# Kernel tuning notes

Hardware: AMD Instinct MI355X
Metric: run time of the kernel (lower is better)

Reference implementation:

```python
import jax, jax.numpy as jnp
import numpy as np

NP_CONST = 48.0  # Np in the original code


def dft_matrices(freq=48, time=512):
    # A[t, f] = exp(-2j*pi*t*f/time)/sqrt(time), split into re/im, shape [time, freq]
    t = np.arange(time)[:, None]
    f = np.arange(freq)[None, :]
    ang = -2.0 * np.pi * t * f / time
    scale = 1.0 / np.sqrt(time)
    return (np.cos(ang) * scale).astype(np.float32), (np.sin(ang) * scale).astype(np.float32)


def _mm(xr, xi, wr, wi):
    # complex matmul: (xr + i xi) @ (wr + i wi)
    return xr @ wr - xi @ wi, xr @ wi + xi @ wr


def _act(R, sigma, theta):
    # scaled soft-threshold (standard LAMP shrinkage); returns f and df/dR
    lam = theta[0] * sigma
    mag = jnp.abs(R)
    shr = jnp.maximum(mag - lam, 0.0)
    f = theta[1] * jnp.sign(R) * shr
    df = theta[1] * (mag > lam).astype(R.dtype)
    return f, df


def setup_inputs() -> dict:
    key = jax.random.key(0)
    L, B = 8, 8192
    dre, dim = dft_matrices(48, 512)
    u = jax.random.normal(key, (B, 48, 2), dtype=jnp.float32)
    # per-layer params initialized to the DFT matrices (as in LAMP_layer.__init__)
    A_re = jnp.broadcast_to(jnp.asarray(dre), (L, 512, 48)).copy()
    A_im = jnp.broadcast_to(jnp.asarray(dim), (L, 512, 48)).copy()
    theta = jnp.broadcast_to(jnp.array([1.0, 1.0, -1.0], dtype=jnp.float32), (L, 3)).copy()
    return {"u": u, "A_re": A_re, "A_im": A_im, "theta": theta,
            "DFT_re": jnp.asarray(dre), "DFT_im": jnp.asarray(dim)}


def _lamp_forward(u, A_re, A_im, theta, DFT_re, DFT_im):
    u_re, u_im = u[:, :, 0], u[:, :, 1]          # [B, 48]
    B = u_re.shape[0]
    z_re, z_im = u_re, u_im
    H_re = jnp.zeros((B, 512), dtype=u.dtype)
    H_im = jnp.zeros((B, 512), dtype=u.dtype)

    def layer(carry, params):
        z_re, z_im, H_re, H_im = carry
        Are, Aim, th = params                      # [512,48], [512,48], [3]
        # Z = z @ A.T : [B,48] x [48,512]
        Z_re, Z_im = _mm(z_re, z_im, Are.T, Aim.T)
        R_re = H_re + Z_re
        R_im = H_im + Z_im
        sigma = jnp.sqrt(jnp.sum(z_re * z_re) + jnp.sum(z_im * z_im)) / jnp.sqrt(NP_CONST)
        Hn_re, d_re = _act(R_re, sigma, th)
        Hn_im, d_im = _act(R_im, sigma, th)
        b_re = d_re.sum() / NP_CONST
        b_im = d_im.sum() / NP_CONST
        # h_hat = H_hat @ A : [B,512] x [512,48]
        h_re, h_im = _mm(Hn_re, Hn_im, Are, Aim)
        zn_re = u_re - h_re + b_re * z_re
        zn_im = u_im - h_im + b_im * z_im
        return (zn_re, zn_im, Hn_re, Hn_im), None

    (z_re, z_im, H_re, H_im), _ = jax.lax.scan(layer, (z_re, z_im, H_re, H_im),
                                               (A_re, A_im, theta))
    h_re, h_im = _mm(H_re, H_im, DFT_re, DFT_im)   # [B, 48]
    return jnp.stack((h_re, h_im), axis=2)          # [B, 48, 2]


def reference(u, A_re, A_im, theta, DFT_re, DFT_im):
    return _lamp_forward(u, A_re, A_im, theta, DFT_re, DFT_im)
```

## Files before the change

kernel.cpp:

```cpp
#include <hip/hip_runtime.h>
#include <hip/hip_bf16.h>
#include <math.h>

#define B_   8192
#define F_   48
#define T_   512
#define L_   8
#define NBLK 512
#define THR  512
#define NW   8
#define RPB  16
#define HST  520
#define ZS   52

typedef unsigned short ushort_t;
typedef unsigned int   uint_t;
typedef __attribute__((ext_vector_type(8))) short short8;
typedef __attribute__((ext_vector_type(4))) float f32x4;

#define MFMA(a,b,c) __builtin_amdgcn_mfma_f32_16x16x32_bf16(a,b,c,0,0,0)

__device__ inline ushort_t f2bf(float x) {
    __hip_bfloat16 h = __float2bfloat16(x);
    return *reinterpret_cast<ushort_t*>(&h);
}
__device__ inline float bf2f(ushort_t x) {
    __hip_bfloat16 h;
    *reinterpret_cast<ushort_t*>(&h) = x;
    return __bfloat162float(h);
}
__device__ inline short8 negbf(short8 v) {
    short8 r;
    #pragma unroll
    for (int i = 0; i < 8; ++i) r[i] = v[i] ^ (short)0x8000;
    return r;
}
__device__ inline short8 pack8(float4 a, float4 b) {
    short8 r;
    r[0]=(short)f2bf(a.x); r[1]=(short)f2bf(a.y); r[2]=(short)f2bf(a.z); r[3]=(short)f2bf(a.w);
    r[4]=(short)f2bf(b.x); r[5]=(short)f2bf(b.y); r[6]=(short)f2bf(b.z); r[7]=(short)f2bf(b.w);
    return r;
}

__device__ inline float blk_sum(float v, float* red8) {
    #pragma unroll
    for (int s = 32; s > 0; s >>= 1) v += __shfl_xor(v, s, 64);
    __syncthreads();
    if ((threadIdx.x & 63) == 0) red8[threadIdx.x >> 6] = v;
    __syncthreads();
    float t = 0.f;
    #pragma unroll
    for (int w = 0; w < NW; ++w) t += red8[w];
    return t;
}

__device__ inline void bar_add(uint_t* cnt, int blk) {
    __hip_atomic_fetch_add(&cnt[(blk & 15) * 32], 1u, __ATOMIC_RELEASE, __HIP_MEMORY_SCOPE_AGENT);
}
__device__ inline void bar_wait(uint_t* cnt, uint_t tgt) {
    if (threadIdx.x == 0) {
        for (;;) {
            uint_t s = 0;
            #pragma unroll
            for (int i = 0; i < 16; ++i)
                s += __hip_atomic_load(&cnt[i * 32], __ATOMIC_RELAXED, __HIP_MEMORY_SCOPE_AGENT);
            if (s >= tgt) break;
            __builtin_amdgcn_s_sleep(2);
        }
        (void)__hip_atomic_load(&cnt[0], __ATOMIC_ACQUIRE, __HIP_MEMORY_SCOPE_AGENT);
    }
    __syncthreads();
}
__device__ inline float aload(const float* p) {
    return __hip_atomic_load(p, __ATOMIC_RELAXED, __HIP_MEMORY_SCOPE_AGENT);
}
__device__ inline void astore(float* p, float v) {
    __hip_atomic_store(p, v, __ATOMIC_RELAXED, __HIP_MEMORY_SCOPE_AGENT);
}

__device__ inline uint_t act2(uint_t v, float lam, float th1, float& cnt_) {
    float lo = __uint_as_float(v << 16);
    float hi = __uint_as_float(v & 0xffff0000u);
    float ml = fabsf(lo), mh = fabsf(hi);
    float fl = th1 * copysignf(fmaxf(ml - lam, 0.f), lo);
    float fh = th1 * copysignf(fmaxf(mh - lam, 0.f), hi);
    cnt_ += ((ml > lam) ? 1.f : 0.f) + ((mh > lam) ? 1.f : 0.f);
    return ((uint_t)f2bf(fl)) | (((uint_t)f2bf(fh)) << 16);
}

__global__ __launch_bounds__(256) void k_pre(
    const float* __restrict__ Ar, const float* __restrict__ Ai,
    const float* __restrict__ Dr, const float* __restrict__ Di,
    ushort_t* __restrict__ Afr, ushort_t* __restrict__ Afi,
    ushort_t* __restrict__ Atr, ushort_t* __restrict__ Ati,
    ushort_t* __restrict__ Dfr, ushort_t* __restrict__ Dfi,
    uint_t* __restrict__ cnt)
{
    const int gt = blockIdx.x * 256 + threadIdx.x;
    const int gs = gridDim.x * 256;
    if (gt < 512) cnt[gt] = 0u;
    for (int idx = gt; idx < L_ * 32768; idx += gs) {
        int j = idx & 7, rest = idx >> 3;
        int mm = rest & 15; rest >>= 4;
        int qq = rest & 3;  rest >>= 2;
        int k2 = rest & 1;  rest >>= 1;
        int tile = rest & 31;
        int l = rest >> 5;
        int t = tile * 16 + mm, k = k2 * 32 + qq * 8 + j;
        float vr = 0.f, vi = 0.f;
        if (k < 48) { int g = l * 24576 + t * 48 + k; vr = Ar[g]; vi = Ai[g]; }
        Afr[idx] = f2bf(vr); Afi[idx] = f2bf(vi);
    }
    for (int idx = gt; idx < L_ * 24576; idx += gs) {
        int j = idx & 7, rest = idx >> 3;
        int mm = rest & 15; rest >>= 4;
        int qq = rest & 3;  rest >>= 2;
        int ks = rest & 15; rest >>= 4;
        int ft = rest % 3;
        int l = rest / 3;
        int f = ft * 16 + mm, k = ks * 32 + qq * 8 + j;
        int g = l * 24576 + k * 48 + f;
        Atr[idx] = f2bf(Ar[g]); Ati[idx] = f2bf(Ai[g]);
    }
    for (int idx = gt; idx < 24576; idx += gs) {
        int j = idx & 7, rest = idx >> 3;
        int mm = rest & 15; rest >>= 4;
        int qq = rest & 3;  rest >>= 2;
        int ks = rest & 15;
        int ft = rest >> 4;
        int f = ft * 16 + mm, k = ks * 32 + qq * 8 + j;
        Dfr[idx] = f2bf(Dr[k * 48 + f]); Dfi[idx] = f2bf(Di[k * 48 + f]);
    }
}

__global__ __launch_bounds__(THR, 4) void k_lamp(
    const float* __restrict__ u,
    const ushort_t* __restrict__ Afr, const ushort_t* __restrict__ Afi,
    const ushort_t* __restrict__ Atr, const ushort_t* __restrict__ Ati,
    const ushort_t* __restrict__ Dfr, const ushort_t* __restrict__ Dfi,
    const float* __restrict__ th,
    float* part_sig, float* part_r, float* part_i, uint_t* cnt,
    float* __restrict__ out)
{
    extern __shared__ char dyn[];
    float*    pR   = (float*)dyn;
    float*    pI   = pR + 4 * 3 * 16 * 17;
    float*    zreL = pI + 4 * 3 * 16 * 17;
    float*    zimL = zreL + RPB * ZS;
    float*    red8 = zimL + RPB * ZS;
    ushort_t* HreL = (ushort_t*)(red8 + 16);
    ushort_t* HimL = HreL + RPB * HST;

    const int tid = threadIdx.x, blk = blockIdx.x;
    const int row0 = blk * RPB;
    const int wave = tid >> 6, lane = tid & 63;
    const int quad = lane >> 4, m = lane & 15;
    const int kq = wave;
    const float2* u2 = (const float2*)u;
    uint_t tgt = 0;

    float acc = 0.f;
    #pragma unroll
    for (int k2 = 0; k2 < 2; ++k2) {
        int j = tid + k2 * THR;
        if (j < RPB * F_) {
            int r = j / 48, c = j - r * 48;
            float2 v = u2[(row0 + r) * 48 + c];
            zreL[r * ZS + c] = v.x; zimL[r * ZS + c] = v.y;
            acc += v.x * v.x + v.y * v.y;
        }
    }
    float s0 = blk_sum(acc, red8);
    if (tid == 0) { astore(&part_sig[blk], s0); bar_add(cnt, blk); }
    tgt += NBLK;

    for (int l = 0; l < L_; ++l) {
        const float* zpr = zreL + m * ZS;
        const float* zpi = zimL + m * ZS;
        short8 zr0 = pack8(*(const float4*)(zpr + quad * 8), *(const float4*)(zpr + quad * 8 + 4));
        short8 zi0 = pack8(*(const float4*)(zpi + quad * 8), *(const float4*)(zpi + quad * 8 + 4));
        short8 zr1 = {0,0,0,0,0,0,0,0}, zi1 = {0,0,0,0,0,0,0,0};
        if (quad < 2) {
            zr1 = pack8(*(const float4*)(zpr + 32 + quad * 8), *(const float4*)(zpr + 36 + quad * 8));
            zi1 = pack8(*(const float4*)(zpi + 32 + quad * 8), *(const float4*)(zpi + 36 + quad * 8));
        }
        short8 zin0 = negbf(zi0), zin1 = negbf(zi1);

        const ushort_t* Aflr = Afr + (size_t)l * 32768;
        const ushort_t* Afli = Afi + (size_t)l * 32768;
        #pragma unroll
        for (int ct = 0; ct < 4; ++ct) {
            const int tile = wave * 4 + ct;
            const ushort_t* rp = Aflr + (size_t)(tile * 2) * 512 + lane * 8;
            const ushort_t* ip = Afli + (size_t)(tile * 2) * 512 + lane * 8;
            short8 ar0 = *(const short8*)rp;
            short8 ar1 = *(const short8*)(rp + 512);
            short8 ai0 = *(const short8*)ip;
            short8 ai1 = *(const short8*)(ip + 512);
            f32x4 accR = {0.f,0.f,0.f,0.f}, accI = {0.f,0.f,0.f,0.f};
            accR = MFMA(zr0, ar0, accR);
            accR = MFMA(zr1, ar1, accR);
            accR = MFMA(zin0, ai0, accR);
            accR = MFMA(zin1, ai1, accR);
            accI = MFMA(zr0, ai0, accI);
            accI = MFMA(zr1, ai1, accI);
            accI = MFMA(zi0, ar0, accI);
            accI = MFMA(zi1, ar1, accI);
            const int t = tile * 16 + m;
            #pragma unroll
            for (int reg = 0; reg < 4; ++reg) {
                const int lr = quad * 4 + reg;
                float Rr = accR[reg], Ri = accI[reg];
                if (l > 0) { Rr += bf2f(HreL[lr * HST + t]); Ri += bf2f(HimL[lr * HST + t]); }
                HreL[lr * HST + t] = f2bf(Rr);
                HimL[lr * HST + t] = f2bf(Ri);
            }
        }

        bar_wait(cnt, tgt);
        float ssum = blk_sum(aload(&part_sig[tid]), red8);
        const float lam = th[l * 3] * sqrtf(ssum * (1.0f / 48.0f));
        const float th1 = th[l * 3 + 1];

        float cr = 0.f, ci = 0.f;
        uint4* Hr4 = (uint4*)HreL;
        uint4* Hi4 = (uint4*)HimL;
        #pragma unroll
        for (int k2 = 0; k2 < 2; ++k2) {
            int j = tid + k2 * THR;
            int r = j >> 6, c4 = j & 63;
            uint4* pr = Hr4 + r * 65 + c4;
            uint4* pi = Hi4 + r * 65 + c4;
            uint4 xr = *pr, xi = *pi;
            xr.x = act2(xr.x, lam, th1, cr); xr.y = act2(xr.y, lam, th1, cr);
            xr.z = act2(xr.z, lam, th1, cr); xr.w = act2(xr.w, lam, th1, cr);
            xi.x = act2(xi.x, lam, th1, ci); xi.y = act2(xi.y, lam, th1, ci);
            xi.z = act2(xi.z, lam, th1, ci); xi.w = act2(xi.w, lam, th1, ci);
            *pr = xr; *pi = xi;
        }

        if (l == L_ - 1) { __syncthreads(); break; }

        float csr = blk_sum(cr, red8);
        if (tid == 0) astore(&part_r[blk], csr);
        float csi = blk_sum(ci, red8);
        if (tid == 0) { astore(&part_i[blk], csi); bar_add(cnt, blk); }
        tgt += NBLK;

        const ushort_t* Atlr = Atr + (size_t)l * 24576;
        const ushort_t* Atli = Ati + (size_t)l * 24576;
        f32x4 aR[3], aI[3];
        #pragma unroll
        for (int q = 0; q < 3; ++q) { aR[q] = (f32x4){0,0,0,0}; aI[q] = (f32x4){0,0,0,0}; }
        #pragma unroll
        for (int ks = 0; ks < 2; ++ks) {
            const int ksa = kq * 2 + ks;
            const int k0 = ksa * 32 + quad * 8;
            short8 hr = *(const short8*)&HreL[m * HST + k0];
            short8 hi = *(const short8*)&HimL[m * HST + k0];
            short8 hin = negbf(hi);
            #pragma unroll
            for (int ft = 0; ft < 3; ++ft) {
                short8 br = *(const short8*)(Atlr + (size_t)((ft * 16 + ksa) * 64 + lane) * 8);
                short8 bi = *(const short8*)(Atli + (size_t)((ft * 16 + ksa) * 64 + lane) * 8);
                aR[ft] = MFMA(hr, br, aR[ft]);
                aR[ft] = MFMA(hin, bi, aR[ft]);
                aI[ft] = MFMA(hr, bi, aI[ft]);
                aI[ft] = MFMA(hi, br, aI[ft]);
            }
        }
        {
            const int s = kq & 3;
            if (kq < 4) {
                #pragma unroll
                for (int ft = 0; ft < 3; ++ft)
                    #pragma unroll
                    for (int reg = 0; reg < 4; ++reg) {
                        pR[((s * 3 + ft) * 16 + quad * 4 + reg) * 17 + m] = aR[ft][reg];
                        pI[((s * 3 + ft) * 16 + quad * 4 + reg) * 17 + m] = aI[ft][reg];
                    }
            }
            __syncthreads();
            if (kq >= 4) {
                #pragma unroll
                for (int ft = 0; ft < 3; ++ft)
                    #pragma unroll
                    for (int reg = 0; reg < 4; ++reg) {
                        pR[((s * 3 + ft) * 16 + quad * 4 + reg) * 17 + m] += aR[ft][reg];
                        pI[((s * 3 + ft) * 16 + quad * 4 + reg) * 17 + m] += aI[ft][reg];
                    }
            }
        }

        bar_wait(cnt, tgt);
        float bsr = blk_sum(aload(&part_r[tid]), red8);
        float bsi = blk_sum(aload(&part_i[tid]), red8);
        const float bre = th1 * bsr * (1.0f / 48.0f);
        const float bim = th1 * bsi * (1.0f / 48.0f);

        float nrm = 0.f;
        #pragma unroll
        for (int k2 = 0; k2 < 2; ++k2) {
            int j = tid + k2 * THR;
            if (j < RPB * F_) {
                int r = j / 48, f = j - r * 48;
                int lr = r & 15, ft = f >> 4, c = f & 15;
                float hR = 0.f, hI = 0.f;
                #pragma unroll
                for (int q = 0; q < 4; ++q) {
                    hR += pR[((q * 3 + ft) * 16 + lr) * 17 + c];
                    hI += pI[((q * 3 + ft) * 16 + lr) * 17 + c];
                }
                float2 uv = u2[(row0 + r) * 48 + f];
                float zr = zreL[r * ZS + f], zi = zimL[r * ZS + f];
                float znr = uv.x - hR + bre * zr;
                float zni = uv.y - hI + bim * zi;
                zreL[r * ZS + f] = znr; zimL[r * ZS + f] = zni;
                nrm += znr * znr + zni * zni;
            }
        }
        float ns = blk_sum(nrm, red8);
        if (tid == 0) { astore(&part_sig[blk], ns); bar_add(cnt, blk); }
        tgt += NBLK;
    }

    f32x4 fR[3], fI[3];
    #pragma unroll
    for (int q = 0; q < 3; ++q) { fR[q] = (f32x4){0,0,0,0}; fI[q] = (f32x4){0,0,0,0}; }
    #pragma unroll
    for (int ks = 0; ks < 2; ++ks) {
        const int ksa = kq * 2 + ks;
        const int k0 = ksa * 32 + quad * 8;
        short8 hr = *(const short8*)&HreL[m * HST + k0];
        short8 hi = *(const short8*)&HimL[m * HST + k0];
        short8 hin = negbf(hi);
        #pragma unroll
        for (int ft = 0; ft < 3; ++ft) {
            short8 br = *(const short8*)(Dfr + (size_t)((ft * 16 + ksa) * 64 + lane) * 8);
            short8 bi = *(const short8*)(Dfi + (size_t)((ft * 16 + ksa) * 64 + lane) * 8);
            fR[ft] = MFMA(hr, br, fR[ft]);
            fR[ft] = MFMA(hin, bi, fR[ft]);
            fI[ft] = MFMA(hr, bi, fI[ft]);
            fI[ft] = MFMA(hi, br, fI[ft]);
        }
    }
    {
        const int s = kq & 3;
        if (kq < 4) {
            #pragma unroll
            for (int ft = 0; ft < 3; ++ft)
                #pragma unroll
                for (int reg = 0; reg < 4; ++reg) {
                    pR[((s * 3 + ft) * 16 + quad * 4 + reg) * 17 + m] = fR[ft][reg];
                    pI[((s * 3 + ft) * 16 + quad * 4 + reg) * 17 + m] = fI[ft][reg];
                }
        }
        __syncthreads();
        if (kq >= 4) {
            #pragma unroll
            for (int ft = 0; ft < 3; ++ft)
                #pragma unroll
                for (int reg = 0; reg < 4; ++reg) {
                    pR[((s * 3 + ft) * 16 + quad * 4 + reg) * 17 + m] += fR[ft][reg];
                    pI[((s * 3 + ft) * 16 + quad * 4 + reg) * 17 + m] += fI[ft][reg];
                }
        }
    }
    __syncthreads();
    float2* out2 = (float2*)out;
    #pragma unroll
    for (int k2 = 0; k2 < 2; ++k2) {
        int j = tid + k2 * THR;
        if (j < RPB * F_) {
            int r = j / 48, f = j - r * 48;
            int lr = r & 15, ft = f >> 4, c = f & 15;
            float hR = 0.f, hI = 0.f;
            #pragma unroll
            for (int q = 0; q < 4; ++q) {
                hR += pR[((q * 3 + ft) * 16 + lr) * 17 + c];
                hI += pI[((q * 3 + ft) * 16 + lr) * 17 + c];
            }
            out2[(row0 + r) * 48 + f] = make_float2(hR, hI);
        }
    }
}

extern "C" void kernel_launch(void* const* d_in, const int* in_sizes, int n_in,
                              void* d_out, int out_size, void* d_ws, size_t ws_size,
                              hipStream_t stream) {
    (void)in_sizes; (void)n_in; (void)out_size; (void)ws_size;
    const float* u  = (const float*)d_in[0];
    const float* Ar = (const float*)d_in[1];
    const float* Ai = (const float*)d_in[2];
    const float* th = (const float*)d_in[3];
    const float* Dr = (const float*)d_in[4];
    const float* Di = (const float*)d_in[5];
    float* out = (float*)d_out;

    char* p = (char*)d_ws;
    auto alloc = [&](size_t bytes) -> char* {
        char* r = p;
        p += (bytes + 255) & ~(size_t)255;
        return r;
    };
    float*    part_sig = (float*)alloc(NBLK * 4);
    float*    part_r   = (float*)alloc(NBLK * 4);
    float*    part_i   = (float*)alloc(NBLK * 4);
    uint_t*   cnt      = (uint_t*)alloc(512 * 4);
    ushort_t* Afr = (ushort_t*)alloc((size_t)L_ * 32768 * 2);
    ushort_t* Afi = (ushort_t*)alloc((size_t)L_ * 32768 * 2);
    ushort_t* Atr = (ushort_t*)alloc((size_t)L_ * 24576 * 2);
    ushort_t* Ati = (ushort_t*)alloc((size_t)L_ * 24576 * 2);
    ushort_t* Dfr = (ushort_t*)alloc((size_t)24576 * 2);
    ushort_t* Dfi = (ushort_t*)alloc((size_t)24576 * 2);

    k_pre<<<256, 256, 0, stream>>>(Ar, Ai, Dr, Di, Afr, Afi, Atr, Ati, Dfr, Dfi, cnt);

    const uint_t lds_bytes = 66112;
    hipFuncSetAttribute((const void*)k_lamp,
                        hipFuncAttributeMaxDynamicSharedMemorySize, (int)lds_bytes);
    void* args[] = { (void*)&u, (void*)&Afr, (void*)&Afi, (void*)&Atr, (void*)&Ati,
                     (void*)&Dfr, (void*)&Dfi, (void*)&th,
                     (void*)&part_sig, (void*)&part_r, (void*)&part_i,
                     (void*)&cnt, (void*)&out };
    hipLaunchCooperativeKernel((void*)k_lamp, dim3(NBLK), dim3(THR), args,
                               lds_bytes, stream);
}
```

Baseline: 309.5 us.

## Merge per-layer grid barriers by computing next sigma algebraically from partial sums

Removes one of the two grid-wide barriers per layer. Each block now publishes the partial sums of d^2, d·z and z^2 together with the derivative counts, and every block expands the next-layer norm of z = d + b*z from those scalars. The forward GEMM for layer 0 runs before the first barrier wait, and the block size is halved to 256 threads with 4 waves, each handling twice the tiles, so two blocks fit per CU. The trade-offs are less intra-block parallelism and a small rounding difference because the norm is computed from expanded sums instead of directly.

Measured after the change: 292.1 us. 1.06x faster.

```diff
diff --git a/kernel.cpp b/kernel.cpp
--- a/kernel.cpp
+++ b/kernel.cpp
@@ -7,8 +7,8 @@
 #define T_   512
 #define L_   8
 #define NBLK 512
-#define THR  512
-#define NW   8
+#define THR  256
+#define NW   4
 #define RPB  16
 #define HST  520
 #define ZS   52
@@ -42,16 +42,17 @@
     return r;
 }
 
-__device__ inline float blk_sum(float v, float* red8) {
+template<int NQ>
+__device__ inline void reduce_vals(float* v, float* redL, int wave, int lane) {
     #pragma unroll
-    for (int s = 32; s > 0; s >>= 1) v += __shfl_xor(v, s, 64);
+    for (int s = 32; s > 0; s >>= 1)
+        #pragma unroll
+        for (int q = 0; q < NQ; ++q) v[q] += __shfl_xor(v[q], s, 64);
     __syncthreads();
-    if ((threadIdx.x & 63) == 0) red8[threadIdx.x >> 6] = v;
+    if (lane == 0)
+        #pragma unroll
+        for (int q = 0; q < NQ; ++q) redL[q * NW + wave] = v[q];
     __syncthreads();
-    float t = 0.f;
-    #pragma unroll
-    for (int w = 0; w < NW; ++w) t += red8[w];
-    return t;
 }
 
 __device__ inline void bar_add(uint_t* cnt, int blk) {
@@ -133,22 +134,67 @@
     }
 }
 
-__global__ __launch_bounds__(THR, 4) void k_lamp(
+__device__ inline void fwd_gemm(const ushort_t* Aflr, const ushort_t* Afli,
+    const float* zreL, const float* zimL, ushort_t* HreL, ushort_t* HimL,
+    int wave, int lane, int quad, int m, bool addH)
+{
+    const float* zpr = zreL + m * ZS;
+    const float* zpi = zimL + m * ZS;
+    short8 zr0 = pack8(*(const float4*)(zpr + quad * 8), *(const float4*)(zpr + quad * 8 + 4));
+    short8 zi0 = pack8(*(const float4*)(zpi + quad * 8), *(const float4*)(zpi + quad * 8 + 4));
+    short8 zr1 = {0,0,0,0,0,0,0,0}, zi1 = {0,0,0,0,0,0,0,0};
+    if (quad < 2) {
+        zr1 = pack8(*(const float4*)(zpr + 32 + quad * 8), *(const float4*)(zpr + 36 + quad * 8));
+        zi1 = pack8(*(const float4*)(zpi + 32 + quad * 8), *(const float4*)(zpi + 36 + quad * 8));
+    }
+    short8 zin0 = negbf(zi0), zin1 = negbf(zi1);
+    #pragma unroll
+    for (int ct = 0; ct < 8; ++ct) {
+        const int tile = wave * 8 + ct;
+        const ushort_t* rp = Aflr + (size_t)(tile * 2) * 512 + lane * 8;
+        const ushort_t* ip = Afli + (size_t)(tile * 2) * 512 + lane * 8;
+        short8 ar0 = *(const short8*)rp;
+        short8 ar1 = *(const short8*)(rp + 512);
+        short8 ai0 = *(const short8*)ip;
+        short8 ai1 = *(const short8*)(ip + 512);
+        f32x4 accR = {0.f,0.f,0.f,0.f}, accI = {0.f,0.f,0.f,0.f};
+        accR = MFMA(zr0, ar0, accR);
+        accR = MFMA(zr1, ar1, accR);
+        accR = MFMA(zin0, ai0, accR);
+        accR = MFMA(zin1, ai1, accR);
+        accI = MFMA(zr0, ai0, accI);
+        accI = MFMA(zr1, ai1, accI);
+        accI = MFMA(zi0, ar0, accI);
+        accI = MFMA(zi1, ar1, accI);
+        const int t = tile * 16 + m;
+        #pragma unroll
+        for (int reg = 0; reg < 4; ++reg) {
+            const int lr = quad * 4 + reg;
+            float Rr = accR[reg], Ri = accI[reg];
+            if (addH) { Rr += bf2f(HreL[lr * HST + t]); Ri += bf2f(HimL[lr * HST + t]); }
+            HreL[lr * HST + t] = f2bf(Rr);
+            HimL[lr * HST + t] = f2bf(Ri);
+        }
+    }
+    __syncthreads();
+}
+
+__global__ __launch_bounds__(THR, 2) void k_lamp(
     const float* __restrict__ u,
     const ushort_t* __restrict__ Afr, const ushort_t* __restrict__ Afi,
     const ushort_t* __restrict__ Atr, const ushort_t* __restrict__ Ati,
     const ushort_t* __restrict__ Dfr, const ushort_t* __restrict__ Dfi,
     const float* __restrict__ th,
-    float* part_sig, float* part_r, float* part_i, uint_t* cnt,
+    float* part, uint_t* cnt,
     float* __restrict__ out)
 {
     extern __shared__ char dyn[];
     float*    pR   = (float*)dyn;
-    float*    pI   = pR + 4 * 3 * 16 * 17;
-    float*    zreL = pI + 4 * 3 * 16 * 17;
+    float*    pI   = pR + 2 * 3 * 16 * 17;
+    float*    zreL = pI + 2 * 3 * 16 * 17;
     float*    zimL = zreL + RPB * ZS;
-    float*    red8 = zimL + RPB * ZS;
-    ushort_t* HreL = (ushort_t*)(red8 + 16);
+    float*    redL = zimL + RPB * ZS;
+    ushort_t* HreL = (ushort_t*)(redL + 32);
     ushort_t* HimL = HreL + RPB * HST;
 
     const int tid = threadIdx.x, blk = blockIdx.x;
@@ -157,121 +203,89 @@
     const int quad = lane >> 4, m = lane & 15;
     const int kq = wave;
     const float2* u2 = (const float2*)u;
-    uint_t tgt = 0;
-
-    float acc = 0.f;
-    #pragma unroll
-    for (int k2 = 0; k2 < 2; ++k2) {
-        int j = tid + k2 * THR;
-        if (j < RPB * F_) {
+    uint_t tgt = NBLK;
+
+    {
+        float acc = 0.f;
+        #pragma unroll
+        for (int k3 = 0; k3 < 3; ++k3) {
+            int j = tid + k3 * THR;
             int r = j / 48, c = j - r * 48;
             float2 v = u2[(row0 + r) * 48 + c];
             zreL[r * ZS + c] = v.x; zimL[r * ZS + c] = v.y;
             acc += v.x * v.x + v.y * v.y;
         }
-    }
-    float s0 = blk_sum(acc, red8);
-    if (tid == 0) { astore(&part_sig[blk], s0); bar_add(cnt, blk); }
-    tgt += NBLK;
-
+        float v[1] = {acc};
+        reduce_vals<1>(v, redL, wave, lane);
+        if (tid == 0) {
+            float t0 = redL[0] + redL[1] + redL[2] + redL[3];
+            astore(&part[blk * 8], t0);
+        }
+        __syncthreads();
+        if (tid == 0) bar_add(cnt, blk);
+    }
+
+    fwd_gemm(Afr, Afi, zreL, zimL, HreL, HimL, wave, lane, quad, m, false);
+
+    bar_wait(cnt, tgt);
+    float lam, th1;
+    {
+        float v[1];
+        v[0] = aload(&part[tid * 8]) + aload(&part[(tid + 256) * 8]);
+        reduce_vals<1>(v, redL, wave, lane);
+        float sig2 = redL[0] + redL[1] + redL[2] + redL[3];
+        lam = th[0] * sqrtf(sig2 * (1.0f / 48.0f));
+        th1 = th[1];
+    }
+
+    float dR[3], dI[3];
     for (int l = 0; l < L_; ++l) {
-        const float* zpr = zreL + m * ZS;
-        const float* zpi = zimL + m * ZS;
-        short8 zr0 = pack8(*(const float4*)(zpr + quad * 8), *(const float4*)(zpr + quad * 8 + 4));
-        short8 zi0 = pack8(*(const float4*)(zpi + quad * 8), *(const float4*)(zpi + quad * 8 + 4));
-        short8 zr1 = {0,0,0,0,0,0,0,0}, zi1 = {0,0,0,0,0,0,0,0};
-        if (quad < 2) {
-            zr1 = pack8(*(const float4*)(zpr + 32 + quad * 8), *(const float4*)(zpr + 36 + quad * 8));
-            zi1 = pack8(*(const float4*)(zpi + 32 + quad * 8), *(const float4*)(zpi + 36 + quad * 8));
-        }
-        short8 zin0 = negbf(zi0), zin1 = negbf(zi1);
-
-        const ushort_t* Aflr = Afr + (size_t)l * 32768;
-        const ushort_t* Afli = Afi + (size_t)l * 32768;
-        #pragma unroll
-        for (int ct = 0; ct < 4; ++ct) {
-            const int tile = wave * 4 + ct;
-            const ushort_t* rp = Aflr + (size_t)(tile * 2) * 512 + lane * 8;
-            const ushort_t* ip = Afli + (size_t)(tile * 2) * 512 + lane * 8;
-            short8 ar0 = *(const short8*)rp;
-            short8 ar1 = *(const short8*)(rp + 512);
-            short8 ai0 = *(const short8*)ip;
-            short8 ai1 = *(const short8*)(ip + 512);
-            f32x4 accR = {0.f,0.f,0.f,0.f}, accI = {0.f,0.f,0.f,0.f};
-            accR = MFMA(zr0, ar0, accR);
-            accR = MFMA(zr1, ar1, accR);
-            accR = MFMA(zin0, ai0, accR);
-            accR = MFMA(zin1, ai1, accR);
-            accI = MFMA(zr0, ai0, accI);
-            accI = MFMA(zr1, ai1, accI);
-            accI = MFMA(zi0, ar0, accI);
-            accI = MFMA(zi1, ar1, accI);
-            const int t = tile * 16 + m;
-            #pragma unroll
-            for (int reg = 0; reg < 4; ++reg) {
-                const int lr = quad * 4 + reg;
-                float Rr = accR[reg], Ri = accI[reg];
-                if (l > 0) { Rr += bf2f(HreL[lr * HST + t]); Ri += bf2f(HimL[lr * HST + t]); }
-                HreL[lr * HST + t] = f2bf(Rr);
-                HimL[lr * HST + t] = f2bf(Ri);
-            }
-        }
-
-        bar_wait(cnt, tgt);
-        float ssum = blk_sum(aload(&part_sig[tid]), red8);
-        const float lam = th[l * 3] * sqrtf(ssum * (1.0f / 48.0f));
-        const float th1 = th[l * 3 + 1];
-
         float cr = 0.f, ci = 0.f;
-        uint4* Hr4 = (uint4*)HreL;
-        uint4* Hi4 = (uint4*)HimL;
-        #pragma unroll
-        for (int k2 = 0; k2 < 2; ++k2) {
-            int j = tid + k2 * THR;
-            int r = j >> 6, c4 = j & 63;
-            uint4* pr = Hr4 + r * 65 + c4;
-            uint4* pi = Hi4 + r * 65 + c4;
-            uint4 xr = *pr, xi = *pi;
-            xr.x = act2(xr.x, lam, th1, cr); xr.y = act2(xr.y, lam, th1, cr);
-            xr.z = act2(xr.z, lam, th1, cr); xr.w = act2(xr.w, lam, th1, cr);
-            xi.x = act2(xi.x, lam, th1, ci); xi.y = act2(xi.y, lam, th1, ci);
-            xi.z = act2(xi.z, lam, th1, ci); xi.w = act2(xi.w, lam, th1, ci);
-            *pr = xr; *pi = xi;
-        }
-
-        if (l == L_ - 1) { __syncthreads(); break; }
-
-        float csr = blk_sum(cr, red8);
-        if (tid == 0) astore(&part_r[blk], csr);
-        float csi = blk_sum(ci, red8);
-        if (tid == 0) { astore(&part_i[blk], csi); bar_add(cnt, blk); }
-        tgt += NBLK;
-
-        const ushort_t* Atlr = Atr + (size_t)l * 24576;
-        const ushort_t* Atli = Ati + (size_t)l * 24576;
-        f32x4 aR[3], aI[3];
-        #pragma unroll
-        for (int q = 0; q < 3; ++q) { aR[q] = (f32x4){0,0,0,0}; aI[q] = (f32x4){0,0,0,0}; }
-        #pragma unroll
-        for (int ks = 0; ks < 2; ++ks) {
-            const int ksa = kq * 2 + ks;
-            const int k0 = ksa * 32 + quad * 8;
-            short8 hr = *(const short8*)&HreL[m * HST + k0];
-            short8 hi = *(const short8*)&HimL[m * HST + k0];
-            short8 hin = negbf(hi);
-            #pragma unroll
-            for (int ft = 0; ft < 3; ++ft) {
-                short8 br = *(const short8*)(Atlr + (size_t)((ft * 16 + ksa) * 64 + lane) * 8);
-                short8 bi = *(const short8*)(Atli + (size_t)((ft * 16 + ksa) * 64 + lane) * 8);
-                aR[ft] = MFMA(hr, br, aR[ft]);
-                aR[ft] = MFMA(hin, bi, aR[ft]);
-                aI[ft] = MFMA(hr, bi, aI[ft]);
-                aI[ft] = MFMA(hi, br, aI[ft]);
-            }
-        }
         {
-            const int s = kq & 3;
-            if (kq < 4) {
+            uint4* Hr4 = (uint4*)HreL;
+            uint4* Hi4 = (uint4*)HimL;
+            #pragma unroll
+            for (int k4 = 0; k4 < 4; ++k4) {
+                int j = tid + k4 * THR;
+                int r = j >> 6, c4 = j & 63;
+                uint4* pr = Hr4 + r * 65 + c4;
+                uint4* pi = Hi4 + r * 65 + c4;
+                uint4 xr = *pr, xi = *pi;
+                xr.x = act2(xr.x, lam, th1, cr); xr.y = act2(xr.y, lam, th1, cr);
+                xr.z = act2(xr.z, lam, th1, cr); xr.w = act2(xr.w, lam, th1, cr);
+                xi.x = act2(xi.x, lam, th1, ci); xi.y = act2(xi.y, lam, th1, ci);
+                xi.z = act2(xi.z, lam, th1, ci); xi.w = act2(xi.w, lam, th1, ci);
+                *pr = xr; *pi = xi;
+            }
+        }
+        __syncthreads();
+        if (l == L_ - 1) break;
+
+        {
+            const ushort_t* Atlr = Atr + (size_t)l * 24576;
+            const ushort_t* Atli = Ati + (size_t)l * 24576;
+            f32x4 aR[3], aI[3];
+            #pragma unroll
+            for (int q = 0; q < 3; ++q) { aR[q] = (f32x4){0,0,0,0}; aI[q] = (f32x4){0,0,0,0}; }
+            #pragma unroll
+            for (int ks = 0; ks < 4; ++ks) {
+                const int ksa = kq * 4 + ks;
+                const int k0 = ksa * 32 + quad * 8;
+                short8 hr = *(const short8*)&HreL[m * HST + k0];
+                short8 hi = *(const short8*)&HimL[m * HST + k0];
+                short8 hin = negbf(hi);
+                #pragma unroll
+                for (int ft = 0; ft < 3; ++ft) {
+                    short8 br = *(const short8*)(Atlr + (size_t)((ft * 16 + ksa) * 64 + lane) * 8);
+                    short8 bi = *(const short8*)(Atli + (size_t)((ft * 16 + ksa) * 64 + lane) * 8);
+                    aR[ft] = MFMA(hr, br, aR[ft]);
+                    aR[ft] = MFMA(hin, bi, aR[ft]);
+                    aI[ft] = MFMA(hr, bi, aI[ft]);
+                    aI[ft] = MFMA(hi, br, aI[ft]);
+                }
+            }
+            const int s = kq & 1;
+            if (kq < 2) {
                 #pragma unroll
                 for (int ft = 0; ft < 3; ++ft)
                     #pragma unroll
@@ -281,7 +295,7 @@
                     }
             }
             __syncthreads();
-            if (kq >= 4) {
+            if (kq >= 2) {
                 #pragma unroll
                 for (int ft = 0; ft < 3; ++ft)
                     #pragma unroll
@@ -290,63 +304,91 @@
                         pI[((s * 3 + ft) * 16 + quad * 4 + reg) * 17 + m] += aI[ft][reg];
                     }
             }
-        }
-
+            __syncthreads();
+        }
+
+        float S1 = 0.f, S2r = 0.f, S2i = 0.f, S3r = 0.f, S3i = 0.f;
+        #pragma unroll
+        for (int k3 = 0; k3 < 3; ++k3) {
+            int j = tid + k3 * THR;
+            int r = j / 48, f = j - r * 48;
+            int ft = f >> 4, c = f & 15;
+            float hR = pR[(ft * 16 + r) * 17 + c] + pR[((3 + ft) * 16 + r) * 17 + c];
+            float hI = pI[(ft * 16 + r) * 17 + c] + pI[((3 + ft) * 16 + r) * 17 + c];
+            float2 uv = u2[(row0 + r) * 48 + f];
+            float zr = zreL[r * ZS + f], zi = zimL[r * ZS + f];
+            float dr = uv.x - hR, di = uv.y - hI;
+            dR[k3] = dr; dI[k3] = di;
+            S1  += dr * dr + di * di;
+            S2r += dr * zr; S2i += di * zi;
+            S3r += zr * zr; S3i += zi * zi;
+        }
+        {
+            float v[7] = {cr, ci, S1, S2r, S2i, S3r, S3i};
+            reduce_vals<7>(v, redL, wave, lane);
+            if (tid < 7) {
+                float t0 = redL[tid * NW] + redL[tid * NW + 1] + redL[tid * NW + 2] + redL[tid * NW + 3];
+                astore(&part[blk * 8 + tid], t0);
+            }
+            __syncthreads();
+            if (tid == 0) bar_add(cnt, blk);
+            tgt += NBLK;
+        }
         bar_wait(cnt, tgt);
-        float bsr = blk_sum(aload(&part_r[tid]), red8);
-        float bsi = blk_sum(aload(&part_i[tid]), red8);
-        const float bre = th1 * bsr * (1.0f / 48.0f);
-        const float bim = th1 * bsi * (1.0f / 48.0f);
-
-        float nrm = 0.f;
-        #pragma unroll
-        for (int k2 = 0; k2 < 2; ++k2) {
-            int j = tid + k2 * THR;
-            if (j < RPB * F_) {
-                int r = j / 48, f = j - r * 48;
-                int lr = r & 15, ft = f >> 4, c = f & 15;
-                float hR = 0.f, hI = 0.f;
-                #pragma unroll
-                for (int q = 0; q < 4; ++q) {
-                    hR += pR[((q * 3 + ft) * 16 + lr) * 17 + c];
-                    hI += pI[((q * 3 + ft) * 16 + lr) * 17 + c];
-                }
-                float2 uv = u2[(row0 + r) * 48 + f];
-                float zr = zreL[r * ZS + f], zi = zimL[r * ZS + f];
-                float znr = uv.x - hR + bre * zr;
-                float zni = uv.y - hI + bim * zi;
-                zreL[r * ZS + f] = znr; zimL[r * ZS + f] = zni;
-                nrm += znr * znr + zni * zni;
-            }
-        }
-        float ns = blk_sum(nrm, red8);
-        if (tid == 0) { astore(&part_sig[blk], ns); bar_add(cnt, blk); }
-        tgt += NBLK;
-    }
-
-    f32x4 fR[3], fI[3];
-    #pragma unroll
-    for (int q = 0; q < 3; ++q) { fR[q] = (f32x4){0,0,0,0}; fI[q] = (f32x4){0,0,0,0}; }
-    #pragma unroll
-    for (int ks = 0; ks < 2; ++ks) {
-        const int ksa = kq * 2 + ks;
-        const int k0 = ksa * 32 + quad * 8;
-        short8 hr = *(const short8*)&HreL[m * HST + k0];
-        short8 hi = *(const short8*)&HimL[m * HST + k0];
-        short8 hin = negbf(hi);
-        #pragma unroll
-        for (int ft = 0; ft < 3; ++ft) {
-            short8 br = *(const short8*)(Dfr + (size_t)((ft * 16 + ksa) * 64 + lane) * 8);
-            short8 bi = *(const short8*)(Dfi + (size_t)((ft * 16 + ksa) * 64 + lane) * 8);
-            fR[ft] = MFMA(hr, br, fR[ft]);
-            fR[ft] = MFMA(hin, bi, fR[ft]);
-            fI[ft] = MFMA(hr, bi, fI[ft]);
-            fI[ft] = MFMA(hi, br, fI[ft]);
-        }
-    }
+        float bre, bim;
+        {
+            float v[7];
+            #pragma unroll
+            for (int q = 0; q < 7; ++q)
+                v[q] = aload(&part[tid * 8 + q]) + aload(&part[(tid + 256) * 8 + q]);
+            reduce_vals<7>(v, redL, wave, lane);
+            float tot[7];
+            #pragma unroll
+            for (int q = 0; q < 7; ++q)
+                tot[q] = redL[q * NW] + redL[q * NW + 1] + redL[q * NW + 2] + redL[q * NW + 3];
+            bre = th1 * tot[0] * (1.0f / 48.0f);
+            bim = th1 * tot[1] * (1.0f / 48.0f);
+            float sig2 = tot[2] + 2.f * bre * tot[3] + 2.f * bim * tot[4]
+                       + bre * bre * tot[5] + bim * bim * tot[6];
+            lam = th[(l + 1) * 3] * sqrtf(sig2 * (1.0f / 48.0f));
+            th1 = th[(l + 1) * 3 + 1];
+        }
+        #pragma unroll
+        for (int k3 = 0; k3 < 3; ++k3) {
+            int j = tid + k3 * THR;
+            int r = j / 48, f = j - r * 48;
+            float zr = zreL[r * ZS + f], zi = zimL[r * ZS + f];
+            zreL[r * ZS + f] = dR[k3] + bre * zr;
+            zimL[r * ZS + f] = dI[k3] + bim * zi;
+        }
+        __syncthreads();
+        fwd_gemm(Afr + (size_t)(l + 1) * 32768, Afi + (size_t)(l + 1) * 32768,
+                 zreL, zimL, HreL, HimL, wave, lane, quad, m, true);
+    }
+
     {
-        const int s = kq & 3;
-        if (kq < 4) {
+        f32x4 fR[3], fI[3];
+        #pragma unroll
+        for (int q = 0; q < 3; ++q) { fR[q] = (f32x4){0,0,0,0}; fI[q] = (f32x4){0,0,0,0}; }
+        #pragma unroll
+        for (int ks = 0; ks < 4; ++ks) {
+            const int ksa = kq * 4 + ks;
+            const int k0 = ksa * 32 + quad * 8;
+            short8 hr = *(const short8*)&HreL[m * HST + k0];
+            short8 hi = *(const short8*)&HimL[m * HST + k0];
+            short8 hin = negbf(hi);
+            #pragma unroll
+            for (int ft = 0; ft < 3; ++ft) {
+                short8 br = *(const short8*)(Dfr + (size_t)((ft * 16 + ksa) * 64 + lane) * 8);
+                short8 bi = *(const short8*)(Dfi + (size_t)((ft * 16 + ksa) * 64 + lane) * 8);
+                fR[ft] = MFMA(hr, br, fR[ft]);
+                fR[ft] = MFMA(hin, bi, fR[ft]);
+                fI[ft] = MFMA(hr, bi, fI[ft]);
+                fI[ft] = MFMA(hi, br, fI[ft]);
+            }
+        }
+        const int s = kq & 1;
+        if (kq < 2) {
             #pragma unroll
             for (int ft = 0; ft < 3; ++ft)
                 #pragma unroll
@@ -356,7 +398,7 @@
                 }
         }
         __syncthreads();
-        if (kq >= 4) {
+        if (kq >= 2) {
             #pragma unroll
             for (int ft = 0; ft < 3; ++ft)
                 #pragma unroll
@@ -365,21 +407,15 @@
                     pI[((s * 3 + ft) * 16 + quad * 4 + reg) * 17 + m] += fI[ft][reg];
                 }
         }
-    }
-    __syncthreads();
-    float2* out2 = (float2*)out;
-    #pragma unroll
-    for (int k2 = 0; k2 < 2; ++k2) {
-        int j = tid + k2 * THR;
-        if (j < RPB * F_) {
+        __syncthreads();
+        float2* out2 = (float2*)out;
+        #pragma unroll
+        for (int k3 = 0; k3 < 3; ++k3) {
+            int j = tid + k3 * THR;
             int r = j / 48, f = j - r * 48;
-            int lr = r & 15, ft = f >> 4, c = f & 15;
-            float hR = 0.f, hI = 0.f;
-            #pragma unroll
-            for (int q = 0; q < 4; ++q) {
-                hR += pR[((q * 3 + ft) * 16 + lr) * 17 + c];
-                hI += pI[((q * 3 + ft) * 16 + lr) * 17 + c];
-            }
+            int ft = f >> 4, c = f & 15;
+            float hR = pR[(ft * 16 + r) * 17 + c] + pR[((3 + ft) * 16 + r) * 17 + c];
+            float hI = pI[(ft * 16 + r) * 17 + c] + pI[((3 + ft) * 16 + r) * 17 + c];
             out2[(row0 + r) * 48 + f] = make_float2(hR, hI);
         }
     }
@@ -403,10 +439,8 @@
         p += (bytes + 255) & ~(size_t)255;
         return r;
     };
-    float*    part_sig = (float*)alloc(NBLK * 4);
-    float*    part_r   = (float*)alloc(NBLK * 4);
-    float*    part_i   = (float*)alloc(NBLK * 4);
-    uint_t*   cnt      = (uint_t*)alloc(512 * 4);
+    float*    part = (float*)alloc((size_t)NBLK * 8 * 4);
+    uint_t*   cnt  = (uint_t*)alloc(512 * 4);
     ushort_t* Afr = (ushort_t*)alloc((size_t)L_ * 32768 * 2);
     ushort_t* Afi = (ushort_t*)alloc((size_t)L_ * 32768 * 2);
     ushort_t* Atr = (ushort_t*)alloc((size_t)L_ * 24576 * 2);
@@ -416,13 +450,12 @@
 
     k_pre<<<256, 256, 0, stream>>>(Ar, Ai, Dr, Di, Afr, Afi, Atr, Ati, Dfr, Dfi, cnt);
 
-    const uint_t lds_bytes = 66112;
+    const uint_t lds_bytes = 53120;
     hipFuncSetAttribute((const void*)k_lamp,
                         hipFuncAttributeMaxDynamicSharedMemorySize, (int)lds_bytes);
     void* args[] = { (void*)&u, (void*)&Afr, (void*)&Afi, (void*)&Atr, (void*)&Ati,
                      (void*)&Dfr, (void*)&Dfi, (void*)&th,
-                     (void*)&part_sig, (void*)&part_r, (void*)&part_i,
-                     (void*)&cnt, (void*)&out };
+                     (void*)&part, (void*)&cnt, (void*)&out };
     hipLaunchCooperativeKernel((void*)k_lamp, dim3(NBLK), dim3(THR), args,
                                lds_bytes, stream);
 }
```
